# Performance work log

Measured on AMD Instinct MI355X. Metric: run time of the kernel, lower is better.

## Reference

```python
import jax, jax.numpy as jnp
import numpy as np

B, S, HID = 2, 2048, 768
NH, HD = 12, 64
WINDOW_HALF = 64  # local_attention // 2
ROPE_THETA = 10000.0  # local_rope_theta (layer_id=1 -> local layer)


def setup_inputs() -> dict:
    key = jax.random.key(0)
    k1, k2, k3 = jax.random.split(key, 3)
    hidden_states = jax.random.normal(k1, (B, S, HID), dtype=jnp.float32)
    Wqkv_w = jax.random.normal(k2, (3 * HID, HID), dtype=jnp.float32) * (1.0 / np.sqrt(HID))
    Wo_w = jax.random.normal(k3, (HID, HID), dtype=jnp.float32) * (1.0 / np.sqrt(HID))
    # additive sliding-window mask: 0 inside +/-WINDOW_HALF band, finfo.min outside
    idx = jnp.arange(S)
    band = jnp.abs(idx[:, None] - idx[None, :]) <= WINDOW_HALF
    neg = jnp.finfo(jnp.float32).min
    sliding_window_mask = jnp.where(band, 0.0, neg)[None, None, :, :].astype(jnp.float32)
    position_ids = jnp.tile(jnp.arange(S, dtype=jnp.int64)[None, :], (B, 1))
    return {
        "hidden_states": hidden_states,
        "Wqkv_w": Wqkv_w,
        "Wo_w": Wo_w,
        "sliding_window_mask": sliding_window_mask,
        "position_ids": position_ids,
    }


def _rotate_half(x):
    x1, x2 = jnp.split(x, 2, axis=-1)
    return jnp.concatenate((-x2, x1), axis=-1)


def _rope_cos_sin(position_ids):
    # inv_freq: [HD//2]
    inv_freq = 1.0 / (ROPE_THETA ** (jnp.arange(0, HD, 2, dtype=jnp.float32) / HD))
    freqs = position_ids.astype(jnp.float32)[:, :, None] * inv_freq[None, None, :]  # [B,S,HD//2]
    emb = jnp.concatenate((freqs, freqs), axis=-1)  # [B,S,HD]
    return jnp.cos(emb), jnp.sin(emb)


def reference(hidden_states, Wqkv_w, Wo_w, sliding_window_mask, position_ids):
    bs, s, _ = hidden_states.shape
    qkv = hidden_states @ Wqkv_w.T  # [B,S,3*HID]
    qkv = qkv.reshape(bs, s, 3, NH, HD)
    # transpose(3,1).unbind(2) -> q,k,v each [B,NH,S,HD]
    qkv = jnp.transpose(qkv, (0, 3, 2, 1, 4))
    q, k, v = qkv[:, :, 0], qkv[:, :, 1], qkv[:, :, 2]
    cos, sin = _rope_cos_sin(position_ids)  # [B,S,HD]
    cos = cos[:, None, :, :].astype(hidden_states.dtype)
    sin = sin[:, None, :, :].astype(hidden_states.dtype)
    q = q * cos + _rotate_half(q) * sin
    k = k * cos + _rotate_half(k) * sin
    scale = 1.0 / np.sqrt(HD)
    scores = jnp.einsum("bhqd,bhkd->bhqk", q, k) * scale + sliding_window_mask
    probs = jax.nn.softmax(scores, axis=-1)
    attn = jnp.einsum("bhqk,bhkd->bhqd", probs, v)  # [B,NH,S,HD]
    attn = jnp.transpose(attn, (0, 2, 1, 3)).reshape(bs, s, NH * HD)
    return attn @ Wo_w.T
```

## Files before the change

kernel.cpp:

```cpp
#include <hip/hip_runtime.h>
#include <hip/hip_bf16.h>
#include <cstdint>

typedef __bf16 bf16_t;
typedef __bf16 bf16x8 __attribute__((ext_vector_type(8)));
typedef float f32x4 __attribute__((ext_vector_type(4)));

#define B_    2
#define S_    2048
#define HID_  768
#define NH_   12
#define HD_   64
#define KDIM_ 768

#define N_HID_  3145728
#define N_WQKV_ 1769472
#define N_WO_   589824

__device__ __forceinline__ void glds16(const bf16_t* g, const bf16_t* lds) {
  __builtin_amdgcn_global_load_lds((const __attribute__((address_space(1))) void*)g,
                                   (__attribute__((address_space(3))) void*)lds,
                                   16, 0, 0);
}

__global__ __launch_bounds__(256) void cvt3_kernel(
    const float* __restrict__ a, const float* __restrict__ b, const float* __restrict__ c,
    bf16_t* __restrict__ da, bf16_t* __restrict__ db, bf16_t* __restrict__ dc)
{
  size_t i = ((size_t)blockIdx.x * 256 + threadIdx.x) * 8;
  const float* s; bf16_t* d; size_t off;
  if (i < N_HID_)                { s = a; d = da; off = i; }
  else if (i < N_HID_ + N_WQKV_) { s = b; d = db; off = i - N_HID_; }
  else                           { s = c; d = dc; off = i - (N_HID_ + N_WQKV_); }
  float4 v0 = *(const float4*)(s + off);
  float4 v1 = *(const float4*)(s + off + 4);
  bf16x8 o;
  o[0] = (bf16_t)v0.x; o[1] = (bf16_t)v0.y; o[2] = (bf16_t)v0.z; o[3] = (bf16_t)v0.w;
  o[4] = (bf16_t)v1.x; o[5] = (bf16_t)v1.y; o[6] = (bf16_t)v1.z; o[7] = (bf16_t)v1.w;
  *(bf16x8*)(d + off) = o;
}

template<int MODE, int BN>
__launch_bounds__(256, 2)
__global__ void gemm_kernel(const bf16_t* __restrict__ A,
                            const bf16_t* __restrict__ Bw,
                            bf16_t* __restrict__ Qo,
                            bf16_t* __restrict__ Ko,
                            bf16_t* __restrict__ Vo,
                            float* __restrict__ outf)
{
  constexpr int NWF = BN / 32;
  __shared__ bf16_t As[128 * 64];
  __shared__ bf16_t Bs[BN * 64];

  const int tid  = threadIdx.x;
  const int w    = tid >> 6;
  const int lane = tid & 63;
  const int wm   = w >> 1, wn = w & 1;
  const int m0   = blockIdx.y * 128;
  const int n0   = blockIdx.x * BN;

  f32x4 acc[4][NWF];
#pragma unroll
  for (int i = 0; i < 4; i++)
#pragma unroll
    for (int j = 0; j < NWF; j++) acc[i][j] = f32x4{0.f, 0.f, 0.f, 0.f};

  const int lr  = lane >> 3;
  const int sub = lane & 7;

  for (int k0 = 0; k0 < KDIM_; k0 += 64) {
#pragma unroll
    for (int q = 0; q < 4; ++q) {
      const int row = q * 32 + w * 8 + lr;
      const int c16 = sub ^ (row & 7);
      glds16(A + (size_t)(m0 + row) * KDIM_ + k0 + c16 * 8, &As[(q * 32 + w * 8) * 64]);
    }
#pragma unroll
    for (int q = 0; q < NWF; ++q) {
      const int row = q * 32 + w * 8 + lr;
      const int c16 = sub ^ (row & 7);
      glds16(Bw + (size_t)(n0 + row) * KDIM_ + k0 + c16 * 8, &Bs[(q * 32 + w * 8) * 64]);
    }
    __syncthreads();

#pragma unroll
    for (int kk = 0; kk < 2; ++kk) {
      const int su = kk * 4 + (lane >> 4);
      bf16x8 af[4], bfr[NWF];
#pragma unroll
      for (int m = 0; m < 4; m++) {
        const int row = wm * 64 + m * 16 + (lane & 15);
        af[m] = *(const bf16x8*)&As[row * 64 + (su ^ (row & 7)) * 8];
      }
#pragma unroll
      for (int n = 0; n < NWF; n++) {
        const int row = wn * (BN / 2) + n * 16 + (lane & 15);
        bfr[n] = *(const bf16x8*)&Bs[row * 64 + (su ^ (row & 7)) * 8];
      }
#pragma unroll
      for (int m = 0; m < 4; m++)
#pragma unroll
        for (int n = 0; n < NWF; n++)
          acc[m][n] = __builtin_amdgcn_mfma_f32_16x16x32_bf16(af[m], bfr[n], acc[m][n], 0, 0, 0);
    }
    __syncthreads();
  }

  const int c = lane & 15;
  if constexpr (MODE == 1) {
#pragma unroll
    for (int m = 0; m < 4; m++)
#pragma unroll
      for (int r = 0; r < 4; r++) {
        const int row = m0 + wm * 64 + m * 16 + (lane >> 4) * 4 + r;
#pragma unroll
        for (int nf = 0; nf < NWF; nf++)
          outf[(size_t)row * HID_ + n0 + wn * (BN / 2) + nf * 16 + c] = acc[m][nf][r];
      }
  } else {
    const int slot  = blockIdx.x * 2 + wn;
    const int which = slot / NH_;
    const int h     = slot % NH_;
    bf16_t* dst = (which == 0) ? Qo : (which == 1 ? Ko : Vo);
    const float NL = -13.287712379549449f / 32.0f;
    const float invf0 = exp2f((float)c * NL);
    const float invf1 = exp2f((float)(16 + c) * NL);
#pragma unroll
    for (int m = 0; m < 4; m++)
#pragma unroll
      for (int r = 0; r < 4; r++) {
        const int row = m0 + wm * 64 + m * 16 + (lane >> 4) * 4 + r;
        const int b = row >> 11, s = row & 2047;
        const size_t base = ((size_t)(b * NH_ + h) * S_ + s) * HD_;
        if (which == 2) {
#pragma unroll
          for (int nf = 0; nf < 4; nf++)
            dst[base + nf * 16 + c] = (bf16_t)acc[m][nf][r];
        } else {
#pragma unroll
          for (int nf = 0; nf < 2; nf++) {
            float sn, cs;
            __sincosf((float)s * (nf ? invf1 : invf0), &sn, &cs);
            const float x1 = acc[m][nf][r], x2 = acc[m][nf + 2][r];
            dst[base + nf * 16 + c]      = (bf16_t)(x1 * cs - x2 * sn);
            dst[base + 32 + nf * 16 + c] = (bf16_t)(x2 * cs + x1 * sn);
          }
        }
      }
  }
}

__launch_bounds__(128, 4)
__global__ void attn_kernel(const bf16_t* __restrict__ Qw,
                            const bf16_t* __restrict__ Kw,
                            const bf16_t* __restrict__ Vw,
                            bf16_t* __restrict__ Ob)
{
  __shared__ bf16_t Vt[64 * 184];
  __shared__ bf16_t Pl[2][16 * 168];

  const int tid  = threadIdx.x;
  const int w    = tid >> 6;
  const int lane = tid & 63;
  const int bxq  = blockIdx.x;
  const int h    = blockIdx.y, b = blockIdx.z;
  const size_t base = (size_t)(b * NH_ + h) * S_ * HD_;
  const int kb = bxq * 32 - 64;

  const int i0 = bxq * 32 + w * 16;
  bf16x8 qf[2];
#pragma unroll
  for (int kk = 0; kk < 2; kk++)
    qf[kk] = *(const bf16x8*)(Qw + base + (size_t)(i0 + (lane & 15)) * HD_ + kk * 32 + (lane >> 4) * 8);

  {
#pragma unroll
    for (int it = 0; it < 10; ++it) {
      const int bk = it * 16 + (tid >> 3);
      const int d0 = (tid & 7) * 8;
      int j = kb + bk; j = j < 0 ? 0 : (j > S_ - 1 ? S_ - 1 : j);
      bf16x8 v = *(const bf16x8*)(Vw + base + (size_t)j * HD_ + d0);
#pragma unroll
      for (int e = 0; e < 8; e++) Vt[(d0 + e) * 184 + bk] = v[e];
    }
    for (int idx = tid; idx < 64 * 24; idx += 128) {
      const int d = idx / 24, cc = 160 + idx % 24;
      Vt[d * 184 + cc] = (bf16_t)0.0f;
    }
  }
  __syncthreads();

  f32x4 sc[9];
#pragma unroll
  for (int t = 0; t < 9; t++) sc[t] = f32x4{0.f, 0.f, 0.f, 0.f};
#pragma unroll
  for (int kk = 0; kk < 2; kk++) {
    const int su = kk * 4 + (lane >> 4);
#pragma unroll
    for (int t = 0; t < 9; t++) {
      const int bk = w * 16 + t * 16 + (lane & 15);
      int j = kb + bk; j = j < 0 ? 0 : (j > S_ - 1 ? S_ - 1 : j);
      bf16x8 kf = *(const bf16x8*)(Kw + base + (size_t)j * HD_ + su * 8);
      sc[t] = __builtin_amdgcn_mfma_f32_16x16x32_bf16(qf[kk], kf, sc[t], 0, 0, 0);
    }
  }

  const int c  = lane & 15;
  const int qh = lane >> 4;
  float lrow[4];
#pragma unroll
  for (int r = 0; r < 4; r++) {
    const int i = i0 + qh * 4 + r;
    float mx = -1e30f;
#pragma unroll
    for (int t = 0; t < 9; t++) {
      const int j = kb + w * 16 + t * 16 + c;
      const int dd = j - i;
      const bool valid = (dd >= -64) && (dd <= 64) && (j >= 0) && (j < S_);
      const float v = valid ? sc[t][r] * 0.125f : -1e30f;
      sc[t][r] = v;
      mx = fmaxf(mx, v);
    }
    mx = fmaxf(mx, __shfl_xor(mx, 1, 16));
    mx = fmaxf(mx, __shfl_xor(mx, 2, 16));
    mx = fmaxf(mx, __shfl_xor(mx, 4, 16));
    mx = fmaxf(mx, __shfl_xor(mx, 8, 16));
    float sum = 0.f;
#pragma unroll
    for (int t = 0; t < 9; t++) {
      const float p = __expf(sc[t][r] - mx);
      sc[t][r] = p;
      sum += p;
    }
    sum += __shfl_xor(sum, 1, 16);
    sum += __shfl_xor(sum, 2, 16);
    sum += __shfl_xor(sum, 4, 16);
    sum += __shfl_xor(sum, 8, 16);
    lrow[r] = sum;
  }

#pragma unroll
  for (int t = 0; t < 9; t++)
#pragma unroll
    for (int r = 0; r < 4; r++)
      Pl[w][(qh * 4 + r) * 168 + t * 16 + c] = (bf16_t)sc[t][r];
#pragma unroll
  for (int r = 0; r < 4; r++)
    Pl[w][(qh * 4 + r) * 168 + 144 + c] = (bf16_t)0.0f;
  asm volatile("s_waitcnt lgkmcnt(0)" ::: "memory");
  __builtin_amdgcn_sched_barrier(0);

  f32x4 ao[4];
#pragma unroll
  for (int nf = 0; nf < 4; nf++) ao[nf] = f32x4{0.f, 0.f, 0.f, 0.f};
#pragma unroll
  for (int kc = 0; kc < 5; kc++) {
    bf16x8 pf = *(const bf16x8*)&Pl[w][(lane & 15) * 168 + kc * 32 + (lane >> 4) * 8];
#pragma unroll
    for (int nf = 0; nf < 4; nf++) {
      const int d = nf * 16 + (lane & 15);
      bf16x8 vf = *(const bf16x8*)&Vt[d * 184 + w * 16 + kc * 32 + (lane >> 4) * 8];
      ao[nf] = __builtin_amdgcn_mfma_f32_16x16x32_bf16(pf, vf, ao[nf], 0, 0, 0);
    }
  }

#pragma unroll
  for (int r = 0; r < 4; r++) {
    const float inv = 1.0f / lrow[r];
    const int srow = i0 + qh * 4 + r;
    const size_t orow = ((size_t)(b * S_ + srow)) * HID_ + h * HD_;
#pragma unroll
    for (int nf = 0; nf < 4; nf++)
      Ob[orow + nf * 16 + c] = (bf16_t)(ao[nf][r] * inv);
  }
}

extern "C" void kernel_launch(void* const* d_in, const int* in_sizes, int n_in,
                              void* d_out, int out_size, void* d_ws, size_t ws_size,
                              hipStream_t stream) {
  const float* hidden_f = (const float*)d_in[0];
  const float* wqkv_f   = (const float*)d_in[1];
  const float* wo_f     = (const float*)d_in[2];

  bf16_t* ws = (bf16_t*)d_ws;
  size_t off = 0;
  bf16_t* Hb    = ws + off; off += N_HID_;
  bf16_t* Wqkvb = ws + off; off += N_WQKV_;
  bf16_t* Wob   = ws + off; off += N_WO_;
  const size_t E = (size_t)B_ * NH_ * S_ * HD_;
  bf16_t* Q    = ws + off; off += E;
  bf16_t* K    = ws + off; off += E;
  bf16_t* V    = ws + off; off += E;
  bf16_t* ABUF = ws + off; off += E;
  float*  out  = (float*)d_out;

  cvt3_kernel<<<dim3((N_HID_ + N_WQKV_ + N_WO_) / (256 * 8)), dim3(256), 0, stream>>>(
      hidden_f, wqkv_f, wo_f, Hb, Wqkvb, Wob);
  gemm_kernel<0, 128><<<dim3(18, 32), dim3(256), 0, stream>>>(Hb, Wqkvb, Q, K, V, nullptr);
  attn_kernel<<<dim3(64, 12, 2), dim3(128), 0, stream>>>(Q, K, V, ABUF);
  gemm_kernel<1, 64><<<dim3(12, 32), dim3(256), 0, stream>>>(ABUF, Wob, nullptr, nullptr, nullptr, out);
}
```

Before: 68.98 us.

## Double-buffer GEMM K loop, retile out-proj, XOR-swizzle attention LDS tiles

The GEMM kernel now double-buffers its LDS tiles, issuing the async global-to-LDS loads for the next K slice before computing the current one, so load latency overlaps with MFMA work. The output-projection GEMM uses 64x64 tiles with twice as many blocks in M, which adds parallelism. The attention kernel's transposed V and P LDS buffers switch from padded strides to an XOR-swizzled 192-wide layout with vectorised zero fills, aimed at cutting bank conflicts. Doubling LDS for the GEMM buffers may reduce occupancy.

```diff
diff --git a/kernel.cpp b/kernel.cpp
--- a/kernel.cpp
+++ b/kernel.cpp
@@ -40,7 +40,7 @@
   *(bf16x8*)(d + off) = o;
 }
 
-template<int MODE, int BN>
+template<int MODE, int BM, int BN>
 __launch_bounds__(256, 2)
 __global__ void gemm_kernel(const bf16_t* __restrict__ A,
                             const bf16_t* __restrict__ Bw,
@@ -49,71 +49,84 @@
                             bf16_t* __restrict__ Vo,
                             float* __restrict__ outf)
 {
-  constexpr int NWF = BN / 32;
-  __shared__ bf16_t As[128 * 64];
-  __shared__ bf16_t Bs[BN * 64];
+  constexpr int MACC = BM / 32;
+  constexpr int NWF  = BN / 32;
+  constexpr int NT   = KDIM_ / 64;
+  __shared__ bf16_t As[2][BM * 64];
+  __shared__ bf16_t Bs[2][BN * 64];
 
   const int tid  = threadIdx.x;
   const int w    = tid >> 6;
   const int lane = tid & 63;
   const int wm   = w >> 1, wn = w & 1;
-  const int m0   = blockIdx.y * 128;
+  const int m0   = blockIdx.y * BM;
   const int n0   = blockIdx.x * BN;
-
-  f32x4 acc[4][NWF];
-#pragma unroll
-  for (int i = 0; i < 4; i++)
+  const int lr   = lane >> 3;
+  const int sub  = lane & 7;
+
+  f32x4 acc[MACC][NWF];
+#pragma unroll
+  for (int i = 0; i < MACC; i++)
 #pragma unroll
     for (int j = 0; j < NWF; j++) acc[i][j] = f32x4{0.f, 0.f, 0.f, 0.f};
 
-  const int lr  = lane >> 3;
-  const int sub = lane & 7;
-
-  for (int k0 = 0; k0 < KDIM_; k0 += 64) {
-#pragma unroll
-    for (int q = 0; q < 4; ++q) {
+  auto STAGE = [&](int buf, int k0) {
+#pragma unroll
+    for (int q = 0; q < MACC; ++q) {
       const int row = q * 32 + w * 8 + lr;
       const int c16 = sub ^ (row & 7);
-      glds16(A + (size_t)(m0 + row) * KDIM_ + k0 + c16 * 8, &As[(q * 32 + w * 8) * 64]);
+      glds16(A + (size_t)(m0 + row) * KDIM_ + k0 + c16 * 8, &As[buf][(q * 32 + w * 8) * 64]);
     }
 #pragma unroll
     for (int q = 0; q < NWF; ++q) {
       const int row = q * 32 + w * 8 + lr;
       const int c16 = sub ^ (row & 7);
-      glds16(Bw + (size_t)(n0 + row) * KDIM_ + k0 + c16 * 8, &Bs[(q * 32 + w * 8) * 64]);
-    }
-    __syncthreads();
-
+      glds16(Bw + (size_t)(n0 + row) * KDIM_ + k0 + c16 * 8, &Bs[buf][(q * 32 + w * 8) * 64]);
+    }
+  };
+
+  auto COMPUTE = [&](int buf) {
 #pragma unroll
     for (int kk = 0; kk < 2; ++kk) {
       const int su = kk * 4 + (lane >> 4);
-      bf16x8 af[4], bfr[NWF];
-#pragma unroll
-      for (int m = 0; m < 4; m++) {
-        const int row = wm * 64 + m * 16 + (lane & 15);
-        af[m] = *(const bf16x8*)&As[row * 64 + (su ^ (row & 7)) * 8];
+      bf16x8 af[MACC], bfr[NWF];
+#pragma unroll
+      for (int m = 0; m < MACC; m++) {
+        const int row = wm * (BM / 2) + m * 16 + (lane & 15);
+        af[m] = *(const bf16x8*)&As[buf][row * 64 + (su ^ (row & 7)) * 8];
       }
 #pragma unroll
       for (int n = 0; n < NWF; n++) {
         const int row = wn * (BN / 2) + n * 16 + (lane & 15);
-        bfr[n] = *(const bf16x8*)&Bs[row * 64 + (su ^ (row & 7)) * 8];
+        bfr[n] = *(const bf16x8*)&Bs[buf][row * 64 + (su ^ (row & 7)) * 8];
       }
 #pragma unroll
-      for (int m = 0; m < 4; m++)
+      for (int m = 0; m < MACC; m++)
 #pragma unroll
         for (int n = 0; n < NWF; n++)
           acc[m][n] = __builtin_amdgcn_mfma_f32_16x16x32_bf16(af[m], bfr[n], acc[m][n], 0, 0, 0);
     }
+  };
+
+  STAGE(0, 0);
+  __syncthreads();
+  int cur = 0;
+#pragma unroll
+  for (int t = 0; t < NT - 1; ++t) {
+    STAGE(cur ^ 1, (t + 1) * 64);
+    COMPUTE(cur);
     __syncthreads();
-  }
+    cur ^= 1;
+  }
+  COMPUTE(cur);
 
   const int c = lane & 15;
   if constexpr (MODE == 1) {
 #pragma unroll
-    for (int m = 0; m < 4; m++)
+    for (int m = 0; m < MACC; m++)
 #pragma unroll
       for (int r = 0; r < 4; r++) {
-        const int row = m0 + wm * 64 + m * 16 + (lane >> 4) * 4 + r;
+        const int row = m0 + wm * (BM / 2) + m * 16 + (lane >> 4) * 4 + r;
 #pragma unroll
         for (int nf = 0; nf < NWF; nf++)
           outf[(size_t)row * HID_ + n0 + wn * (BN / 2) + nf * 16 + c] = acc[m][nf][r];
@@ -127,10 +140,10 @@
     const float invf0 = exp2f((float)c * NL);
     const float invf1 = exp2f((float)(16 + c) * NL);
 #pragma unroll
-    for (int m = 0; m < 4; m++)
+    for (int m = 0; m < MACC; m++)
 #pragma unroll
       for (int r = 0; r < 4; r++) {
-        const int row = m0 + wm * 64 + m * 16 + (lane >> 4) * 4 + r;
+        const int row = m0 + wm * (BM / 2) + m * 16 + (lane >> 4) * 4 + r;
         const int b = row >> 11, s = row & 2047;
         const size_t base = ((size_t)(b * NH_ + h) * S_ + s) * HD_;
         if (which == 2) {
@@ -157,8 +170,8 @@
                             const bf16_t* __restrict__ Vw,
                             bf16_t* __restrict__ Ob)
 {
-  __shared__ bf16_t Vt[64 * 184];
-  __shared__ bf16_t Pl[2][16 * 168];
+  __shared__ bf16_t Vt[64 * 192];
+  __shared__ bf16_t Pl[2][16 * 192];
 
   const int tid  = threadIdx.x;
   const int w    = tid >> 6;
@@ -181,12 +194,16 @@
       const int d0 = (tid & 7) * 8;
       int j = kb + bk; j = j < 0 ? 0 : (j > S_ - 1 ? S_ - 1 : j);
       bf16x8 v = *(const bf16x8*)(Vw + base + (size_t)j * HD_ + d0);
-#pragma unroll
-      for (int e = 0; e < 8; e++) Vt[(d0 + e) * 184 + bk] = v[e];
-    }
-    for (int idx = tid; idx < 64 * 24; idx += 128) {
-      const int d = idx / 24, cc = 160 + idx % 24;
-      Vt[d * 184 + cc] = (bf16_t)0.0f;
+      const int gsw = (((bk >> 3) ^ (tid & 7)) << 3) + (bk & 7);
+#pragma unroll
+      for (int e = 0; e < 8; e++) Vt[(d0 + e) * 192 + gsw] = v[e];
+    }
+    const bf16x8 z8 = {};
+#pragma unroll
+    for (int zz = 0; zz < 2; ++zz) {
+      const int idx = zz * 128 + tid;
+      const int d = idx >> 2, g = 20 + (idx & 3);
+      *(bf16x8*)&Vt[d * 192 + ((g ^ (d >> 3)) << 3)] = z8;
     }
   }
   __syncthreads();
@@ -243,11 +260,16 @@
 #pragma unroll
   for (int t = 0; t < 9; t++)
 #pragma unroll
-    for (int r = 0; r < 4; r++)
-      Pl[w][(qh * 4 + r) * 168 + t * 16 + c] = (bf16_t)sc[t][r];
-#pragma unroll
-  for (int r = 0; r < 4; r++)
-    Pl[w][(qh * 4 + r) * 168 + 144 + c] = (bf16_t)0.0f;
+    for (int r = 0; r < 4; r++) {
+      const int row = qh * 4 + r;
+      const int col = t * 16 + c;
+      Pl[w][row * 192 + (((col >> 3) ^ (row & 7)) << 3) + (col & 7)] = (bf16_t)sc[t][r];
+    }
+  {
+    const bf16x8 z8 = {};
+    const int row = lane & 15, g = 18 + ((lane >> 4) & 1);
+    *(bf16x8*)&Pl[w][row * 192 + ((g ^ (row & 7)) << 3)] = z8;
+  }
   asm volatile("s_waitcnt lgkmcnt(0)" ::: "memory");
   __builtin_amdgcn_sched_barrier(0);
 
@@ -256,11 +278,14 @@
   for (int nf = 0; nf < 4; nf++) ao[nf] = f32x4{0.f, 0.f, 0.f, 0.f};
 #pragma unroll
   for (int kc = 0; kc < 5; kc++) {
-    bf16x8 pf = *(const bf16x8*)&Pl[w][(lane & 15) * 168 + kc * 32 + (lane >> 4) * 8];
+    const int prow = lane & 15;
+    const int Lp = kc * 32 + (lane >> 4) * 8;
+    bf16x8 pf = *(const bf16x8*)&Pl[w][prow * 192 + (((Lp >> 3) ^ (prow & 7)) << 3)];
 #pragma unroll
     for (int nf = 0; nf < 4; nf++) {
       const int d = nf * 16 + (lane & 15);
-      bf16x8 vf = *(const bf16x8*)&Vt[d * 184 + w * 16 + kc * 32 + (lane >> 4) * 8];
+      const int L = w * 16 + Lp;
+      bf16x8 vf = *(const bf16x8*)&Vt[d * 192 + (((L >> 3) ^ (d >> 3)) << 3)];
       ao[nf] = __builtin_amdgcn_mfma_f32_16x16x32_bf16(pf, vf, ao[nf], 0, 0, 0);
     }
   }
@@ -297,7 +322,7 @@
 
   cvt3_kernel<<<dim3((N_HID_ + N_WQKV_ + N_WO_) / (256 * 8)), dim3(256), 0, stream>>>(
       hidden_f, wqkv_f, wo_f, Hb, Wqkvb, Wob);
-  gemm_kernel<0, 128><<<dim3(18, 32), dim3(256), 0, stream>>>(Hb, Wqkvb, Q, K, V, nullptr);
+  gemm_kernel<0, 128, 128><<<dim3(18, 32), dim3(256), 0, stream>>>(Hb, Wqkvb, Q, K, V, nullptr);
   attn_kernel<<<dim3(64, 12, 2), dim3(128), 0, stream>>>(Q, K, V, ABUF);
-  gemm_kernel<1, 64><<<dim3(12, 32), dim3(256), 0, stream>>>(ABUF, Wob, nullptr, nullptr, nullptr, out);
-}
+  gemm_kernel<1, 64, 64><<<dim3(12, 64), dim3(256), 0, stream>>>(ABUF, Wob, nullptr, nullptr, nullptr, out);
+}
```

After: 76.22 us. +10.5%, slower.
